# Optimization experiments

Hardware: AMD Instinct MI355X
Metric: run time of the kernel (lower is better)

The kernel has to match this reference:

```python
import jax, jax.numpy as jnp
import numpy as np

NEG_SLOPE = 0.2


def setup_inputs() -> dict:
    key = jax.random.key(0)
    ks = jax.random.split(key, 5)
    N, E, Din, Dout = 100000, 1600000, 64, 64
    x = jax.random.normal(ks[0], (N, Din), dtype=jnp.float32)
    edge_index = jax.random.randint(ks[1], (2, E), 0, N, dtype=jnp.int64)
    # Glorot-ish scale for weights
    W_l = jax.random.normal(ks[2], (Din, Dout), dtype=jnp.float32) / np.sqrt(Din)
    W_r = jax.random.normal(ks[3], (Din, Dout), dtype=jnp.float32) / np.sqrt(Din)
    att = jax.random.normal(ks[4], (Dout,), dtype=jnp.float32) / np.sqrt(Dout)
    bias = jnp.zeros((Dout,), dtype=jnp.float32)
    return {"x": x, "edge_index": edge_index, "W_l": W_l, "W_r": W_r, "att": att, "bias": bias}


def reference(x, edge_index, W_l, W_r, att, bias):
    N = x.shape[0]
    # PyG GATv2Conv default: add self loops
    loop = jnp.arange(N, dtype=edge_index.dtype)
    src = jnp.concatenate([edge_index[0], loop])  # j (source / message)
    dst = jnp.concatenate([edge_index[1], loop])  # i (target / aggregation)

    x_l = x @ W_l  # [N, Dout] source transform
    x_r = x @ W_r  # [N, Dout] target transform

    # per-edge attention logit: att . LeakyReLU(x_l[j] + x_r[i])
    e = jax.nn.leaky_relu(x_l[src] + x_r[dst], NEG_SLOPE) @ att  # [E+N]

    # segment softmax grouped by destination node
    e_max = jax.ops.segment_max(e, dst, num_segments=N)  # [N]
    e_exp = jnp.exp(e - e_max[dst])
    denom = jax.ops.segment_sum(e_exp, dst, num_segments=N)  # [N]
    alpha = e_exp / denom[dst]  # [E+N]

    # weighted scatter-add aggregation of source features
    out = jax.ops.segment_sum(alpha[:, None] * x_l[src], dst, num_segments=N)
    return out + bias
```

## Files before the change

kernel.cpp:

```cpp
#include <hip/hip_runtime.h>
#include <hip/hip_fp16.h>

#define NEG_SLOPE 0.2f
#define CH 4096
#define UN 16
#define BW 512
#define CAP2 10240

__global__ __launch_bounds__(256) void k_gemm(const float* __restrict__ x,
                                              const float* __restrict__ Wl,
                                              const float* __restrict__ Wr,
                                              __half* __restrict__ xl,
                                              __half* __restrict__ xr, int N) {
    __shared__ float sX[128 * 64];
    __shared__ float sW[64 * 128];
    const int t = threadIdx.x;
    const int B = blockIdx.x * 128;

    for (int f = t; f < 2048; f += 256) {
        const int k = f >> 5, cg = f & 31;
        float4 v;
        if (cg < 16) v = reinterpret_cast<const float4*>(Wl)[k * 16 + cg];
        else         v = reinterpret_cast<const float4*>(Wr)[k * 16 + (cg - 16)];
        reinterpret_cast<float4*>(sW)[f] = v;
    }
    for (int f = t; f < 2048; f += 256) {
        const int r = B + (f >> 4);
        float4 v = {0.f, 0.f, 0.f, 0.f};
        if (r < N) v = reinterpret_cast<const float4*>(x)[(size_t)B * 16 + f];
        reinterpret_cast<float4*>(sX)[f] = v;
    }
    __syncthreads();

    const int cg = t & 31;
    const int g  = t >> 5;

    float4 acc[16];
#pragma unroll
    for (int i = 0; i < 16; i++) acc[i] = make_float4(0.f, 0.f, 0.f, 0.f);

    for (int kk = 0; kk < 64; kk += 4) {
        const float4 w0 = reinterpret_cast<const float4*>(sW)[(kk + 0) * 32 + cg];
        const float4 w1 = reinterpret_cast<const float4*>(sW)[(kk + 1) * 32 + cg];
        const float4 w2 = reinterpret_cast<const float4*>(sW)[(kk + 2) * 32 + cg];
        const float4 w3 = reinterpret_cast<const float4*>(sW)[(kk + 3) * 32 + cg];
#pragma unroll
        for (int i = 0; i < 16; i++) {
            const float4 xv = reinterpret_cast<const float4*>(sX)[(g * 16 + i) * 16 + (kk >> 2)];
            acc[i].x = fmaf(xv.x, w0.x, acc[i].x);
            acc[i].y = fmaf(xv.x, w0.y, acc[i].y);
            acc[i].z = fmaf(xv.x, w0.z, acc[i].z);
            acc[i].w = fmaf(xv.x, w0.w, acc[i].w);
            acc[i].x = fmaf(xv.y, w1.x, acc[i].x);
            acc[i].y = fmaf(xv.y, w1.y, acc[i].y);
            acc[i].z = fmaf(xv.y, w1.z, acc[i].z);
            acc[i].w = fmaf(xv.y, w1.w, acc[i].w);
            acc[i].x = fmaf(xv.z, w2.x, acc[i].x);
            acc[i].y = fmaf(xv.z, w2.y, acc[i].y);
            acc[i].z = fmaf(xv.z, w2.z, acc[i].z);
            acc[i].w = fmaf(xv.z, w2.w, acc[i].w);
            acc[i].x = fmaf(xv.w, w3.x, acc[i].x);
            acc[i].y = fmaf(xv.w, w3.y, acc[i].y);
            acc[i].z = fmaf(xv.w, w3.z, acc[i].z);
            acc[i].w = fmaf(xv.w, w3.w, acc[i].w);
        }
    }

    const int c = cg * 4;
    __half* dstp = (c < 64) ? (xl + c) : (xr + (c - 64));
#pragma unroll
    for (int i = 0; i < 16; i++) {
        const int r = B + g * 16 + i;
        if (r < N) {
            __half2 h01, h23;
            h01.x = __float2half_rn(acc[i].x);
            h01.y = __float2half_rn(acc[i].y);
            h23.x = __float2half_rn(acc[i].z);
            h23.y = __float2half_rn(acc[i].w);
            uint2 u;
            u.x = *reinterpret_cast<unsigned int*>(&h01);
            u.y = *reinterpret_cast<unsigned int*>(&h23);
            *reinterpret_cast<uint2*>(dstp + (size_t)r * 64) = u;
        }
    }
}

__global__ __launch_bounds__(256) void k_part(const int* __restrict__ src,
                                              const int* __restrict__ dst,
                                              int* __restrict__ bcount,
                                              int* __restrict__ part,
                                              int E, int M, int NB) {
    __shared__ int skey[CH];
    __shared__ unsigned char sbkt[CH];
    __shared__ int hist[256];
    __shared__ int lcur[256];
    __shared__ int gofs[256];
    const int t = threadIdx.x;
    const int b = blockIdx.x;
    const int lo = b * CH;
    const int cnt = min(M - lo, CH);

    hist[t] = 0;
    __syncthreads();

    int rs[UN], rd[UN];
#pragma unroll
    for (int u = 0; u < UN; u++) {
        const int k = lo + t + u * 256;
        rd[u] = -1; rs[u] = 0;
        if (k < M) {
            if (k < E) { rs[u] = src[k]; rd[u] = dst[k]; }
            else       { rs[u] = k - E;  rd[u] = rs[u]; }
        }
    }
#pragma unroll
    for (int u = 0; u < UN; u++)
        if (rd[u] >= 0) atomicAdd(&hist[rd[u] >> 9], 1);
    __syncthreads();

    const int h = hist[t];
    lcur[t] = h;
    __syncthreads();
    for (int o = 1; o < 256; o <<= 1) {
        const int v = (t >= o) ? lcur[t - o] : 0;
        __syncthreads();
        lcur[t] += v;
        __syncthreads();
    }
    const int ex = lcur[t] - h;
    int gbase = 0;
    if (t < NB && h > 0) gbase = atomicAdd(&bcount[t], h);
    __syncthreads();
    lcur[t] = ex;
    gofs[t] = t * CAP2 + gbase - ex;
    __syncthreads();

#pragma unroll
    for (int u = 0; u < UN; u++) {
        if (rd[u] >= 0) {
            const int bkt = rd[u] >> 9;
            const int p = atomicAdd(&lcur[bkt], 1);
            skey[p] = (rs[u] << 9) | (rd[u] & 511);
            sbkt[p] = (unsigned char)bkt;
        }
    }
    __syncthreads();

    for (int i = t; i < cnt; i += 256) {
        const int bkt = sbkt[i];
        const int pos = gofs[bkt] + i;
        if (pos - bkt * CAP2 < CAP2) part[pos] = skey[i];
    }
}

__global__ __launch_bounds__(256) void k_bsort(const int* __restrict__ part,
                                               const int* __restrict__ bcount,
                                               int* __restrict__ sedge,
                                               int* __restrict__ off,
                                               int* __restrict__ deg, int N) {
    __shared__ int keys[CAP2];
    __shared__ int outk[CAP2];
    __shared__ int lhist[512];
    __shared__ int lcur[512];
    __shared__ int sh2[256];
    const int t = threadIdx.x;
    const int bkt = blockIdx.x;
    const int base = bkt * CAP2;
    const int n = min(bcount[bkt], CAP2);

    for (int i = t; i < 512; i += 256) lhist[i] = 0;
    __syncthreads();
    for (int i = t; i < n; i += 256) {
        const int k = part[base + i];
        keys[i] = k;
        atomicAdd(&lhist[k & 511], 1);
    }
    __syncthreads();

    const int a0 = lhist[2 * t], a1 = lhist[2 * t + 1];
    const int ps = a0 + a1;
    sh2[t] = ps;
    __syncthreads();
    for (int o = 1; o < 256; o <<= 1) {
        int v = (t >= o) ? sh2[t - o] : 0;
        __syncthreads();
        sh2[t] += v;
        __syncthreads();
    }
    const int ex = sh2[t] - ps;
    lcur[2 * t]     = ex;
    lcur[2 * t + 1] = ex + a0;
    const int d0 = (bkt << 9) + 2 * t;
    if (d0 < N)     { off[d0] = base + ex;          deg[d0] = a0; }
    if (d0 + 1 < N) { off[d0 + 1] = base + ex + a0; deg[d0 + 1] = a1; }
    __syncthreads();

    for (int i = t; i < n; i += 256) {
        const int k = keys[i];
        const int pos = atomicAdd(&lcur[k & 511], 1);
        outk[pos] = k >> 9;
    }
    __syncthreads();
    for (int i = t; i < n; i += 256) sedge[base + i] = outk[i];
}

__global__ void k_fused(const int* __restrict__ offv, const int* __restrict__ degv,
                        const int* __restrict__ sedge, const __half* __restrict__ xl,
                        const __half* __restrict__ xr, const float* __restrict__ att,
                        const float* __restrict__ bias, float* __restrict__ out, int N) {
    const int lane = threadIdx.x & 63;
    const int gl = lane & 15;
    const int q = lane >> 4;
    int wave = (blockIdx.x * blockDim.x + threadIdx.x) >> 6;
    const int nw = (gridDim.x * blockDim.x) >> 6;
    const float4 a = reinterpret_cast<const float4*>(att)[gl];
    const float4 b = reinterpret_cast<const float4*>(bias)[gl];
    for (int i = wave; i < N; i += nw) {
        const int base = offv[i];
        const int dg = degv[i];
        const uint2 xru = reinterpret_cast<const uint2*>(xr + (size_t)i * 64)[gl];
        const float2 r01 = __half22float2(*reinterpret_cast<const __half2*>(&xru.x));
        const float2 r23 = __half22float2(*reinterpret_cast<const __half2*>(&xru.y));
        float s = 0.f;
        float4 acc = {0.f, 0.f, 0.f, 0.f};
        for (int t = q; t < dg; t += 4) {
            const int j = sedge[base + t];
            const uint2 xu = reinterpret_cast<const uint2*>(xl + (size_t)j * 64)[gl];
            const float2 l01 = __half22float2(*reinterpret_cast<const __half2*>(&xu.x));
            const float2 l23 = __half22float2(*reinterpret_cast<const __half2*>(&xu.y));
            float v0 = l01.x + r01.x; v0 = fmaxf(v0, NEG_SLOPE * v0);
            float v1 = l01.y + r01.y; v1 = fmaxf(v1, NEG_SLOPE * v1);
            float v2 = l23.x + r23.x; v2 = fmaxf(v2, NEG_SLOPE * v2);
            float v3 = l23.y + r23.y; v3 = fmaxf(v3, NEG_SLOPE * v3);
            float p = a.x * v0 + a.y * v1 + a.z * v2 + a.w * v3;
            p += __shfl_xor(p, 1, 16);
            p += __shfl_xor(p, 2, 16);
            p += __shfl_xor(p, 4, 16);
            p += __shfl_xor(p, 8, 16);
            const float w = __expf(p);
            s += w;
            acc.x = fmaf(w, l01.x, acc.x);
            acc.y = fmaf(w, l01.y, acc.y);
            acc.z = fmaf(w, l23.x, acc.z);
            acc.w = fmaf(w, l23.y, acc.w);
        }
        s += __shfl_xor(s, 16); s += __shfl_xor(s, 32);
        acc.x += __shfl_xor(acc.x, 16); acc.x += __shfl_xor(acc.x, 32);
        acc.y += __shfl_xor(acc.y, 16); acc.y += __shfl_xor(acc.y, 32);
        acc.z += __shfl_xor(acc.z, 16); acc.z += __shfl_xor(acc.z, 32);
        acc.w += __shfl_xor(acc.w, 16); acc.w += __shfl_xor(acc.w, 32);
        if (q == 0) {
            const float inv = 1.f / s;
            float4 o;
            o.x = fmaf(acc.x, inv, b.x);
            o.y = fmaf(acc.y, inv, b.y);
            o.z = fmaf(acc.z, inv, b.z);
            o.w = fmaf(acc.w, inv, b.w);
            reinterpret_cast<float4*>(out)[(size_t)i * 16 + gl] = o;
        }
    }
}

extern "C" void kernel_launch(void* const* d_in, const int* in_sizes, int n_in,
                              void* d_out, int out_size, void* d_ws, size_t ws_size,
                              hipStream_t stream) {
    const float* x    = (const float*)d_in[0];
    const int*   ei   = (const int*)d_in[1];
    const float* Wl   = (const float*)d_in[2];
    const float* Wr   = (const float*)d_in[3];
    const float* att  = (const float*)d_in[4];
    const float* bias = (const float*)d_in[5];
    float* out = (float*)d_out;

    const int N = in_sizes[0] / 64;
    const int E = in_sizes[1] / 2;
    const int M = E + N;
    const int ng  = (N + 127) / 128;
    const int nch = (M + CH - 1) / CH;
    const int NB  = (N + BW - 1) / BW;

    __half* xl = (__half*)d_ws;
    __half* xr = xl + (size_t)N * 64;
    int* deg    = (int*)(xr + (size_t)N * 64);
    int* off    = deg + N;
    int* bcount = off + N;
    int* part   = bcount + NB;
    int* sedge  = part + (size_t)NB * CAP2;

    hipMemsetAsync(bcount, 0, (size_t)NB * sizeof(int), stream);

    k_gemm<<<ng, 256, 0, stream>>>(x, Wl, Wr, xl, xr, N);
    k_part<<<nch, 256, 0, stream>>>(ei, ei + E, bcount, part, E, M, NB);
    k_bsort<<<NB, 256, 0, stream>>>(part, bcount, sedge, off, deg, N);
    k_fused<<<2048, 256, 0, stream>>>(off, deg, sedge, xl, xr, att, bias, out, N);
}
```

Baseline: 216.9 us.

## Fuse bucket sort into attention aggregation kernel with 256-node buckets

Merges the per-bucket counting sort and the attention/softmax aggregation into one kernel, so sorted source indices stay in shared memory instead of being written to and re-read from global sedge/off/deg arrays. Buckets shrink from 512 to 256 destination nodes (CAP 5120) so each 512-thread block can hold keys and sorted arrays in LDS. The partition kernel now uses 512 histogram bins with a paired scan. Trade-offs: only about 391 blocks of 8 waves each do the gather work, which risks underfilling the GPU compared with the prior persistent 2048-block launch. Per-bucket capacity is tighter, so edges past CAP would be dropped if a bucket overflows.

Measured after the change: 257.1 us. 1.19x slower.

```diff
diff --git a/kernel.cpp b/kernel.cpp
--- a/kernel.cpp
+++ b/kernel.cpp
@@ -4,8 +4,7 @@
 #define NEG_SLOPE 0.2f
 #define CH 4096
 #define UN 16
-#define BW 512
-#define CAP2 10240
+#define CAP 5120
 
 __global__ __launch_bounds__(256) void k_gemm(const float* __restrict__ x,
                                               const float* __restrict__ Wl,
@@ -91,16 +90,17 @@
                                               int* __restrict__ part,
                                               int E, int M, int NB) {
     __shared__ int skey[CH];
-    __shared__ unsigned char sbkt[CH];
-    __shared__ int hist[256];
-    __shared__ int lcur[256];
-    __shared__ int gofs[256];
+    __shared__ unsigned short sbkt[CH];
+    __shared__ int hist[512];
+    __shared__ int lcur[512];
+    __shared__ int gofs[512];
+    __shared__ int sh2[256];
     const int t = threadIdx.x;
     const int b = blockIdx.x;
     const int lo = b * CH;
     const int cnt = min(M - lo, CH);
 
-    hist[t] = 0;
+    hist[t] = 0; hist[t + 256] = 0;
     __syncthreads();
 
     int rs[UN], rd[UN];
@@ -115,33 +115,39 @@
     }
 #pragma unroll
     for (int u = 0; u < UN; u++)
-        if (rd[u] >= 0) atomicAdd(&hist[rd[u] >> 9], 1);
-    __syncthreads();
-
-    const int h = hist[t];
-    lcur[t] = h;
+        if (rd[u] >= 0) atomicAdd(&hist[rd[u] >> 8], 1);
+    __syncthreads();
+
+    const int a0 = hist[2 * t], a1 = hist[2 * t + 1];
+    const int ps = a0 + a1;
+    sh2[t] = ps;
     __syncthreads();
     for (int o = 1; o < 256; o <<= 1) {
-        const int v = (t >= o) ? lcur[t - o] : 0;
-        __syncthreads();
-        lcur[t] += v;
-        __syncthreads();
-    }
-    const int ex = lcur[t] - h;
-    int gbase = 0;
-    if (t < NB && h > 0) gbase = atomicAdd(&bcount[t], h);
-    __syncthreads();
-    lcur[t] = ex;
-    gofs[t] = t * CAP2 + gbase - ex;
+        const int v = (t >= o) ? sh2[t - o] : 0;
+        __syncthreads();
+        sh2[t] += v;
+        __syncthreads();
+    }
+    const int ex = sh2[t] - ps;
+    lcur[2 * t]     = ex;
+    lcur[2 * t + 1] = ex + a0;
+    if (2 * t < NB && a0 > 0) {
+        const int g = atomicAdd(&bcount[2 * t], a0);
+        gofs[2 * t] = 2 * t * CAP + g - ex;
+    }
+    if (2 * t + 1 < NB && a1 > 0) {
+        const int g = atomicAdd(&bcount[2 * t + 1], a1);
+        gofs[2 * t + 1] = (2 * t + 1) * CAP + g - (ex + a0);
+    }
     __syncthreads();
 
 #pragma unroll
     for (int u = 0; u < UN; u++) {
         if (rd[u] >= 0) {
-            const int bkt = rd[u] >> 9;
+            const int bkt = rd[u] >> 8;
             const int p = atomicAdd(&lcur[bkt], 1);
-            skey[p] = (rs[u] << 9) | (rd[u] & 511);
-            sbkt[p] = (unsigned char)bkt;
+            skey[p] = (rs[u] << 8) | (rd[u] & 255);
+            sbkt[p] = (unsigned short)bkt;
         }
     }
     __syncthreads();
@@ -149,82 +155,76 @@
     for (int i = t; i < cnt; i += 256) {
         const int bkt = sbkt[i];
         const int pos = gofs[bkt] + i;
-        if (pos - bkt * CAP2 < CAP2) part[pos] = skey[i];
-    }
-}
-
-__global__ __launch_bounds__(256) void k_bsort(const int* __restrict__ part,
-                                               const int* __restrict__ bcount,
-                                               int* __restrict__ sedge,
-                                               int* __restrict__ off,
-                                               int* __restrict__ deg, int N) {
-    __shared__ int keys[CAP2];
-    __shared__ int outk[CAP2];
-    __shared__ int lhist[512];
-    __shared__ int lcur[512];
+        if (pos - bkt * CAP < CAP) part[pos] = skey[i];
+    }
+}
+
+__global__ __launch_bounds__(512) void k_sf(const int* __restrict__ part,
+                                            const int* __restrict__ bcount,
+                                            const __half* __restrict__ xl,
+                                            const __half* __restrict__ xr,
+                                            const float* __restrict__ att,
+                                            const float* __restrict__ bias,
+                                            float* __restrict__ out, int N) {
+    __shared__ int keys[CAP];
+    __shared__ int sorted[CAP];
+    __shared__ int lhist[256];
+    __shared__ int loff[256];
+    __shared__ int lcur[256];
     __shared__ int sh2[256];
     const int t = threadIdx.x;
     const int bkt = blockIdx.x;
-    const int base = bkt * CAP2;
-    const int n = min(bcount[bkt], CAP2);
-
-    for (int i = t; i < 512; i += 256) lhist[i] = 0;
-    __syncthreads();
-    for (int i = t; i < n; i += 256) {
+    const int base = bkt * CAP;
+    const int n = min(bcount[bkt], CAP);
+
+    if (t < 256) lhist[t] = 0;
+    __syncthreads();
+    for (int i = t; i < n; i += 512) {
         const int k = part[base + i];
         keys[i] = k;
-        atomicAdd(&lhist[k & 511], 1);
-    }
-    __syncthreads();
-
-    const int a0 = lhist[2 * t], a1 = lhist[2 * t + 1];
-    const int ps = a0 + a1;
-    sh2[t] = ps;
+        atomicAdd(&lhist[k & 255], 1);
+    }
+    __syncthreads();
+    if (t < 256) sh2[t] = lhist[t];
     __syncthreads();
     for (int o = 1; o < 256; o <<= 1) {
-        int v = (t >= o) ? sh2[t - o] : 0;
-        __syncthreads();
-        sh2[t] += v;
-        __syncthreads();
-    }
-    const int ex = sh2[t] - ps;
-    lcur[2 * t]     = ex;
-    lcur[2 * t + 1] = ex + a0;
-    const int d0 = (bkt << 9) + 2 * t;
-    if (d0 < N)     { off[d0] = base + ex;          deg[d0] = a0; }
-    if (d0 + 1 < N) { off[d0 + 1] = base + ex + a0; deg[d0 + 1] = a1; }
-    __syncthreads();
-
-    for (int i = t; i < n; i += 256) {
+        int v = 0;
+        if (t < 256 && t >= o) v = sh2[t - o];
+        __syncthreads();
+        if (t < 256) sh2[t] += v;
+        __syncthreads();
+    }
+    if (t < 256) {
+        const int ex = sh2[t] - lhist[t];
+        loff[t] = ex;
+        lcur[t] = ex;
+    }
+    __syncthreads();
+    for (int i = t; i < n; i += 512) {
         const int k = keys[i];
-        const int pos = atomicAdd(&lcur[k & 511], 1);
-        outk[pos] = k >> 9;
-    }
-    __syncthreads();
-    for (int i = t; i < n; i += 256) sedge[base + i] = outk[i];
-}
-
-__global__ void k_fused(const int* __restrict__ offv, const int* __restrict__ degv,
-                        const int* __restrict__ sedge, const __half* __restrict__ xl,
-                        const __half* __restrict__ xr, const float* __restrict__ att,
-                        const float* __restrict__ bias, float* __restrict__ out, int N) {
-    const int lane = threadIdx.x & 63;
+        const int pos = atomicAdd(&lcur[k & 255], 1);
+        sorted[pos] = k >> 8;
+    }
+    __syncthreads();
+
+    const int lane = t & 63;
     const int gl = lane & 15;
     const int q = lane >> 4;
-    int wave = (blockIdx.x * blockDim.x + threadIdx.x) >> 6;
-    const int nw = (gridDim.x * blockDim.x) >> 6;
+    const int w = t >> 6;
     const float4 a = reinterpret_cast<const float4*>(att)[gl];
-    const float4 b = reinterpret_cast<const float4*>(bias)[gl];
-    for (int i = wave; i < N; i += nw) {
-        const int base = offv[i];
-        const int dg = degv[i];
-        const uint2 xru = reinterpret_cast<const uint2*>(xr + (size_t)i * 64)[gl];
+    const float4 bb = reinterpret_cast<const float4*>(bias)[gl];
+    for (int dlo = w * 32; dlo < w * 32 + 32; dlo++) {
+        const int node = (bkt << 8) + dlo;
+        if (node >= N) break;
+        const int eb = loff[dlo];
+        const int dg = lhist[dlo];
+        const uint2 xru = reinterpret_cast<const uint2*>(xr + (size_t)node * 64)[gl];
         const float2 r01 = __half22float2(*reinterpret_cast<const __half2*>(&xru.x));
         const float2 r23 = __half22float2(*reinterpret_cast<const __half2*>(&xru.y));
         float s = 0.f;
         float4 acc = {0.f, 0.f, 0.f, 0.f};
-        for (int t = q; t < dg; t += 4) {
-            const int j = sedge[base + t];
+        for (int tt = q; tt < dg; tt += 4) {
+            const int j = sorted[eb + tt];
             const uint2 xu = reinterpret_cast<const uint2*>(xl + (size_t)j * 64)[gl];
             const float2 l01 = __half22float2(*reinterpret_cast<const __half2*>(&xu.x));
             const float2 l23 = __half22float2(*reinterpret_cast<const __half2*>(&xu.y));
@@ -237,12 +237,12 @@
             p += __shfl_xor(p, 2, 16);
             p += __shfl_xor(p, 4, 16);
             p += __shfl_xor(p, 8, 16);
-            const float w = __expf(p);
-            s += w;
-            acc.x = fmaf(w, l01.x, acc.x);
-            acc.y = fmaf(w, l01.y, acc.y);
-            acc.z = fmaf(w, l23.x, acc.z);
-            acc.w = fmaf(w, l23.y, acc.w);
+            const float wgt = __expf(p);
+            s += wgt;
+            acc.x = fmaf(wgt, l01.x, acc.x);
+            acc.y = fmaf(wgt, l01.y, acc.y);
+            acc.z = fmaf(wgt, l23.x, acc.z);
+            acc.w = fmaf(wgt, l23.y, acc.w);
         }
         s += __shfl_xor(s, 16); s += __shfl_xor(s, 32);
         acc.x += __shfl_xor(acc.x, 16); acc.x += __shfl_xor(acc.x, 32);
@@ -252,11 +252,11 @@
         if (q == 0) {
             const float inv = 1.f / s;
             float4 o;
-            o.x = fmaf(acc.x, inv, b.x);
-            o.y = fmaf(acc.y, inv, b.y);
-            o.z = fmaf(acc.z, inv, b.z);
-            o.w = fmaf(acc.w, inv, b.w);
-            reinterpret_cast<float4*>(out)[(size_t)i * 16 + gl] = o;
+            o.x = fmaf(acc.x, inv, bb.x);
+            o.y = fmaf(acc.y, inv, bb.y);
+            o.z = fmaf(acc.z, inv, bb.z);
+            o.w = fmaf(acc.w, inv, bb.w);
+            reinterpret_cast<float4*>(out)[(size_t)node * 16 + gl] = o;
         }
     }
 }
@@ -277,20 +277,16 @@
     const int M = E + N;
     const int ng  = (N + 127) / 128;
     const int nch = (M + CH - 1) / CH;
-    const int NB  = (N + BW - 1) / BW;
+    const int NB  = (N + 255) / 256;
 
     __half* xl = (__half*)d_ws;
     __half* xr = xl + (size_t)N * 64;
-    int* deg    = (int*)(xr + (size_t)N * 64);
-    int* off    = deg + N;
-    int* bcount = off + N;
+    int* bcount = (int*)(xr + (size_t)N * 64);
     int* part   = bcount + NB;
-    int* sedge  = part + (size_t)NB * CAP2;
 
     hipMemsetAsync(bcount, 0, (size_t)NB * sizeof(int), stream);
 
     k_gemm<<<ng, 256, 0, stream>>>(x, Wl, Wr, xl, xr, N);
     k_part<<<nch, 256, 0, stream>>>(ei, ei + E, bcount, part, E, M, NB);
-    k_bsort<<<NB, 256, 0, stream>>>(part, bcount, sedge, off, deg, N);
-    k_fused<<<2048, 256, 0, stream>>>(off, deg, sedge, xl, xr, att, bias, out, N);
-}
+    k_sf<<<NB, 512, 0, stream>>>(part, bcount, xl, xr, att, bias, out, N);
+}
```

## Split bucket sort into quarter-blocks, fold counter reset into GEMM, unroll gather loop

Applied to the files above, without the earlier changes.

The per-bucket sort kernel now runs four blocks per 512-node bucket. Each block filters the keys for its 128-node quarter and sorts them with smaller shared arrays, which raises parallelism and occupancy. The separate memset of the bucket counters is removed and block 0 of the GEMM zeroes them instead, saving one launch. The fused attention loop handles two edges per iteration to expose more memory-level parallelism. The costs are that each quarter block re-reads the whole bucket, and the fixed QCAP of 2560 per quarter risks overflow on skewed degree distributions.

New measurement: 206.0 us. 5.0% less time.

```diff
diff --git a/kernel.cpp b/kernel.cpp
--- a/kernel.cpp
+++ b/kernel.cpp
@@ -6,16 +6,21 @@
 #define UN 16
 #define BW 512
 #define CAP2 10240
+#define QCAP 2560
 
 __global__ __launch_bounds__(256) void k_gemm(const float* __restrict__ x,
                                               const float* __restrict__ Wl,
                                               const float* __restrict__ Wr,
                                               __half* __restrict__ xl,
-                                              __half* __restrict__ xr, int N) {
+                                              __half* __restrict__ xr,
+                                              int* __restrict__ bcount,
+                                              int NB, int N) {
     __shared__ float sX[128 * 64];
     __shared__ float sW[64 * 128];
     const int t = threadIdx.x;
     const int B = blockIdx.x * 128;
+
+    if (blockIdx.x == 0 && t < NB) bcount[t] = 0;
 
     for (int f = t; f < 2048; f += 256) {
         const int k = f >> 5, cg = f & 31;
@@ -153,55 +158,68 @@
     }
 }
 
-__global__ __launch_bounds__(256) void k_bsort(const int* __restrict__ part,
-                                               const int* __restrict__ bcount,
-                                               int* __restrict__ sedge,
-                                               int* __restrict__ off,
-                                               int* __restrict__ deg, int N) {
-    __shared__ int keys[CAP2];
-    __shared__ int outk[CAP2];
-    __shared__ int lhist[512];
-    __shared__ int lcur[512];
-    __shared__ int sh2[256];
+__global__ __launch_bounds__(256) void k_bsf(const int* __restrict__ part,
+                                             const int* __restrict__ bcount,
+                                             int* __restrict__ sedge,
+                                             int* __restrict__ off,
+                                             int* __restrict__ deg, int N) {
+    __shared__ int skey[QCAP];
+    __shared__ int outk[QCAP];
+    __shared__ int lhist[128];
+    __shared__ int loff[128];
+    __shared__ int lcur[128];
+    __shared__ int sh2[128];
+    __shared__ int scnt;
     const int t = threadIdx.x;
-    const int bkt = blockIdx.x;
-    const int base = bkt * CAP2;
+    const int bkt = blockIdx.x >> 2;
+    const int qt  = blockIdx.x & 3;
+    const int base  = bkt * CAP2;
+    const int qbase = base + qt * QCAP;
     const int n = min(bcount[bkt], CAP2);
 
-    for (int i = t; i < 512; i += 256) lhist[i] = 0;
-    __syncthreads();
+    if (t == 0) scnt = 0;
+    if (t < 128) lhist[t] = 0;
+    __syncthreads();
+
     for (int i = t; i < n; i += 256) {
         const int k = part[base + i];
-        keys[i] = k;
-        atomicAdd(&lhist[k & 511], 1);
-    }
-    __syncthreads();
-
-    const int a0 = lhist[2 * t], a1 = lhist[2 * t + 1];
-    const int ps = a0 + a1;
-    sh2[t] = ps;
-    __syncthreads();
-    for (int o = 1; o < 256; o <<= 1) {
-        int v = (t >= o) ? sh2[t - o] : 0;
+        const int dl = k & 511;
+        if ((dl >> 7) == qt) {
+            const int p = atomicAdd(&scnt, 1);
+            if (p < QCAP) {
+                skey[p] = k;
+                atomicAdd(&lhist[dl & 127], 1);
+            }
+        }
+    }
+    __syncthreads();
+    const int m = min(scnt, QCAP);
+
+    if (t < 128) sh2[t] = lhist[t];
+    __syncthreads();
+    for (int o = 1; o < 128; o <<= 1) {
+        int v = 0;
+        if (t < 128 && t >= o) v = sh2[t - o];
         __syncthreads();
-        sh2[t] += v;
+        if (t < 128) sh2[t] += v;
         __syncthreads();
     }
-    const int ex = sh2[t] - ps;
-    lcur[2 * t]     = ex;
-    lcur[2 * t + 1] = ex + a0;
-    const int d0 = (bkt << 9) + 2 * t;
-    if (d0 < N)     { off[d0] = base + ex;          deg[d0] = a0; }
-    if (d0 + 1 < N) { off[d0 + 1] = base + ex + a0; deg[d0 + 1] = a1; }
-    __syncthreads();
-
-    for (int i = t; i < n; i += 256) {
-        const int k = keys[i];
-        const int pos = atomicAdd(&lcur[k & 511], 1);
+    if (t < 128) {
+        const int ex = sh2[t] - lhist[t];
+        loff[t] = ex;
+        lcur[t] = ex;
+        const int node = (bkt << 9) + (qt << 7) + t;
+        if (node < N) { off[node] = qbase + ex; deg[node] = lhist[t]; }
+    }
+    __syncthreads();
+
+    for (int i = t; i < m; i += 256) {
+        const int k = skey[i];
+        const int pos = atomicAdd(&lcur[k & 127], 1);
         outk[pos] = k >> 9;
     }
     __syncthreads();
-    for (int i = t; i < n; i += 256) sedge[base + i] = outk[i];
+    for (int i = t; i < m; i += 256) sedge[qbase + i] = outk[i];
 }
 
 __global__ void k_fused(const int* __restrict__ offv, const int* __restrict__ degv,
@@ -223,8 +241,44 @@
         const float2 r23 = __half22float2(*reinterpret_cast<const __half2*>(&xru.y));
         float s = 0.f;
         float4 acc = {0.f, 0.f, 0.f, 0.f};
-        for (int t = q; t < dg; t += 4) {
-            const int j = sedge[base + t];
+        int tt = q;
+        for (; tt + 4 < dg; tt += 8) {
+            const int j0 = sedge[base + tt];
+            const int j1 = sedge[base + tt + 4];
+            const uint2 xu0 = reinterpret_cast<const uint2*>(xl + (size_t)j0 * 64)[gl];
+            const uint2 xu1 = reinterpret_cast<const uint2*>(xl + (size_t)j1 * 64)[gl];
+            const float2 l01a = __half22float2(*reinterpret_cast<const __half2*>(&xu0.x));
+            const float2 l23a = __half22float2(*reinterpret_cast<const __half2*>(&xu0.y));
+            const float2 l01b = __half22float2(*reinterpret_cast<const __half2*>(&xu1.x));
+            const float2 l23b = __half22float2(*reinterpret_cast<const __half2*>(&xu1.y));
+            float v0 = l01a.x + r01.x; v0 = fmaxf(v0, NEG_SLOPE * v0);
+            float v1 = l01a.y + r01.y; v1 = fmaxf(v1, NEG_SLOPE * v1);
+            float v2 = l23a.x + r23.x; v2 = fmaxf(v2, NEG_SLOPE * v2);
+            float v3 = l23a.y + r23.y; v3 = fmaxf(v3, NEG_SLOPE * v3);
+            float u0 = l01b.x + r01.x; u0 = fmaxf(u0, NEG_SLOPE * u0);
+            float u1 = l01b.y + r01.y; u1 = fmaxf(u1, NEG_SLOPE * u1);
+            float u2 = l23b.x + r23.x; u2 = fmaxf(u2, NEG_SLOPE * u2);
+            float u3 = l23b.y + r23.y; u3 = fmaxf(u3, NEG_SLOPE * u3);
+            float p0 = a.x * v0 + a.y * v1 + a.z * v2 + a.w * v3;
+            float p1 = a.x * u0 + a.y * u1 + a.z * u2 + a.w * u3;
+            p0 += __shfl_xor(p0, 1, 16);
+            p1 += __shfl_xor(p1, 1, 16);
+            p0 += __shfl_xor(p0, 2, 16);
+            p1 += __shfl_xor(p1, 2, 16);
+            p0 += __shfl_xor(p0, 4, 16);
+            p1 += __shfl_xor(p1, 4, 16);
+            p0 += __shfl_xor(p0, 8, 16);
+            p1 += __shfl_xor(p1, 8, 16);
+            const float w0 = __expf(p0);
+            const float w1 = __expf(p1);
+            s += w0 + w1;
+            acc.x = fmaf(w0, l01a.x, acc.x); acc.x = fmaf(w1, l01b.x, acc.x);
+            acc.y = fmaf(w0, l01a.y, acc.y); acc.y = fmaf(w1, l01b.y, acc.y);
+            acc.z = fmaf(w0, l23a.x, acc.z); acc.z = fmaf(w1, l23b.x, acc.z);
+            acc.w = fmaf(w0, l23a.y, acc.w); acc.w = fmaf(w1, l23b.y, acc.w);
+        }
+        for (; tt < dg; tt += 4) {
+            const int j = sedge[base + tt];
             const uint2 xu = reinterpret_cast<const uint2*>(xl + (size_t)j * 64)[gl];
             const float2 l01 = __half22float2(*reinterpret_cast<const __half2*>(&xu.x));
             const float2 l23 = __half22float2(*reinterpret_cast<const __half2*>(&xu.y));
@@ -287,10 +341,8 @@
     int* part   = bcount + NB;
     int* sedge  = part + (size_t)NB * CAP2;
 
-    hipMemsetAsync(bcount, 0, (size_t)NB * sizeof(int), stream);
-
-    k_gemm<<<ng, 256, 0, stream>>>(x, Wl, Wr, xl, xr, N);
+    k_gemm<<<ng, 256, 0, stream>>>(x, Wl, Wr, xl, xr, bcount, NB, N);
     k_part<<<nch, 256, 0, stream>>>(ei, ei + E, bcount, part, E, M, NB);
-    k_bsort<<<NB, 256, 0, stream>>>(part, bcount, sedge, off, deg, N);
+    k_bsf<<<NB * 4, 256, 0, stream>>>(part, bcount, sedge, off, deg, N);
     k_fused<<<2048, 256, 0, stream>>>(off, deg, sedge, xl, xr, att, bias, out, N);
 }
```
